# Performance work log

Hardware: AMD Instinct MI355X
Metric: run time of the kernel (lower is better)

Reference implementation:

```python
import jax, jax.numpy as jnp
import numpy as np

N_NODES = 100000
N_EDGES = 1200000
D = 64
N_CLASSES = 16
L2_EPS = 1e-12  # F.normalize default eps


def setup_inputs() -> dict:
    key = jax.random.key(0)
    ks = jax.random.split(key, 8)
    x = jax.random.normal(ks[0], (N_NODES, D), dtype=jnp.float32)
    src = jax.random.randint(ks[1], (N_EDGES,), 0, N_NODES, dtype=jnp.int32)
    dst = jax.random.randint(ks[2], (N_EDGES,), 0, N_NODES, dtype=jnp.int32)
    s = 1.0 / np.sqrt(D)
    W0 = jax.random.normal(ks[3], (D, D), dtype=jnp.float32) * s  # stored as [in, out]
    W1 = jax.random.normal(ks[4], (D, D), dtype=jnp.float32) * s
    W2 = jax.random.normal(ks[5], (D, D), dtype=jnp.float32) * s
    W_out = jax.random.normal(ks[6], (D, N_CLASSES), dtype=jnp.float32) * s
    b_out = jnp.zeros((N_CLASSES,), dtype=jnp.float32)
    return {"x": x, "src": src, "dst": dst, "W0": W0, "W1": W1, "W2": W2,
            "W_out": W_out, "b_out": b_out}


def reference(x, src, dst, W0, W1, W2, W_out, b_out):
    n = x.shape[0]
    h = x
    for W in (W0, W1, W2):
        # GINConv sum aggregation (eps=0): h_dst = h + sum over incoming edges
        agg = jax.ops.segment_sum(h[src], dst, num_segments=n)
        # MLP: relu(linear); GraphConv post-activation relu is idempotent on relu output
        h = jax.nn.relu((h + agg) @ W)
    # F.normalize: L2 row normalization with eps clamp
    norm = jnp.linalg.norm(h, axis=1, keepdims=True)
    feat = h / jnp.maximum(norm, L2_EPS)
    out = feat @ W_out + b_out
    return out, feat
```

## Files before the change

kernel.cpp:

```cpp
#include <hip/hip_runtime.h>
#include <hip/hip_fp16.h>

#define N_NODES 100000
#define N_EDGES 1200000
#define D 64
#define N_CLASSES 16
#define NG8  (N_NODES / 8)
#define GRID 2048
#define NXCD 8
#define DRANGE ((N_NODES + NXCD - 1) / NXCD)
#define ESRC_CAP 1900032
#define SENTINEL N_NODES
#define NB_CVT 6250
#define NRB 1024
#define RW 98
#define RCAP 2048
#define K1CH 1024
#define K1B ((N_EDGES / 4 + K1CH - 1) / K1CH)

typedef _Float16 f16x8 __attribute__((ext_vector_type(8)));
typedef float    f32x4 __attribute__((ext_vector_type(4)));

__global__ __launch_bounds__(256) void bucket_nr_kernel(
        const int* __restrict__ src,
        const int* __restrict__ dst,
        int* __restrict__ bcur,
        int* __restrict__ bpk) {
    __shared__ int hist[NRB];
    __shared__ int lofs[NRB + 1];
    __shared__ int gbase[NRB];
    __shared__ int tsum[256];
    __shared__ int pk[K1CH * 4];
    int tid = threadIdx.x;
    for (int i = tid; i < NRB; i += 256) hist[i] = 0;
    __syncthreads();

    int c0 = blockIdx.x * K1CH;
    int bn_rk[4][4], pkv[4][4];
#pragma unroll
    for (int it = 0; it < 4; ++it) {
        int c = c0 + it * 256 + tid;
        if (c < N_EDGES / 4) {
            int4 s4 = ((const int4*)src)[c];
            int4 d4 = ((const int4*)dst)[c];
            int ss[4] = {s4.x, s4.y, s4.z, s4.w};
            int dd[4] = {d4.x, d4.y, d4.z, d4.w};
#pragma unroll
            for (int j = 0; j < 4; ++j) {
                int b = dd[j] / RW;
                int rk = atomicAdd(&hist[b], 1);
                bn_rk[it][j] = (b << 16) | rk;
                pkv[it][j] = (ss[j] << 7) | (dd[j] - b * RW);
            }
        } else {
#pragma unroll
            for (int j = 0; j < 4; ++j) bn_rk[it][j] = -1;
        }
    }
    __syncthreads();
    int b4 = tid * 4;
    int h0 = hist[b4], h1 = hist[b4 + 1], h2 = hist[b4 + 2], h3 = hist[b4 + 3];
    int hs = h0 + h1 + h2 + h3;
    tsum[tid] = hs;
    __syncthreads();
    for (int d = 1; d < 256; d <<= 1) {
        int t = (tid >= d) ? tsum[tid - d] : 0;
        __syncthreads();
        tsum[tid] += t;
        __syncthreads();
    }
    int ex = tsum[tid] - hs;
    lofs[b4] = ex; lofs[b4 + 1] = ex + h0;
    lofs[b4 + 2] = ex + h0 + h1; lofs[b4 + 3] = ex + h0 + h1 + h2;
    if (tid == 255) lofs[NRB] = tsum[255];
    for (int b = tid; b < NRB; b += 256) {
        int cb = hist[b];
        gbase[b] = cb ? atomicAdd(&bcur[b], cb) : 0;
    }
    __syncthreads();
#pragma unroll
    for (int it = 0; it < 4; ++it)
#pragma unroll
        for (int j = 0; j < 4; ++j) {
            int br = bn_rk[it][j];
            if (br >= 0)
                pk[lofs[br >> 16] + (br & 0xffff)] = pkv[it][j];
        }
    __syncthreads();
    int total = lofs[NRB];
    for (int i = tid; i < total; i += 256) {
        int lo = 0, hi = NRB;
        while (hi - lo > 1) {
            int mid = (lo + hi) >> 1;
            if (lofs[mid] <= i) lo = mid; else hi = mid;
        }
        int pos = gbase[lo] + (i - lofs[lo]);
        if (pos < RCAP) bpk[lo * RCAP + pos] = pk[i];
    }
}

__global__ __launch_bounds__(256) void hist_nr_kernel(
        const int* __restrict__ bcur,
        const int* __restrict__ bpk,
        int* __restrict__ cnt) {
    __shared__ int lh[RW];
    int r = blockIdx.x, tid = threadIdx.x;
    if (tid < RW) lh[tid] = 0;
    __syncthreads();
    int nb = min(bcur[r], RCAP);
    const int* p = bpk + r * RCAP;
    for (int i = tid; i < nb; i += 256)
        atomicAdd(&lh[p[i] & 127], 1);
    __syncthreads();
    int n = r * RW + tid;
    if (tid < RW && n < N_NODES) cnt[n] = lh[tid];
}

__global__ void scan_block_kernel(const int* __restrict__ cnt,
                                  int* __restrict__ ofs,
                                  int* __restrict__ partial) {
    __shared__ int s[256];
    int tid = threadIdx.x;
    int i = blockIdx.x * 256 + tid;
    int v = (i < N_NODES) ? ((cnt[i] + 7) & ~7) : 0;
    s[tid] = v;
    __syncthreads();
    for (int d = 1; d < 256; d <<= 1) {
        int t = (tid >= d) ? s[tid - d] : 0;
        __syncthreads();
        s[tid] += t;
        __syncthreads();
    }
    if (i < N_NODES) ofs[i] = s[tid] - v;
    if (tid == 255) partial[blockIdx.x] = s[255];
}

__global__ void scan_partials_kernel(int* __restrict__ partial, int nb) {
    __shared__ int s[512];
    int tid = threadIdx.x;
    int v = (tid < nb) ? partial[tid] : 0;
    s[tid] = v;
    __syncthreads();
    for (int d = 1; d < 512; d <<= 1) {
        int t = (tid >= d) ? s[tid - d] : 0;
        __syncthreads();
        s[tid] += t;
        __syncthreads();
    }
    if (tid < nb) partial[tid] = s[tid] - v;
}

__global__ void scan_add_kernel(int* __restrict__ ofs,
                                const int* __restrict__ partial,
                                const int* __restrict__ cnt,
                                int* __restrict__ esrc) {
    int i = blockIdx.x * 256 + threadIdx.x;
    if (i < N_NODES) {
        int o = ofs[i] + partial[blockIdx.x];
        ofs[i] = o;
        int c = cnt[i], p = (c + 7) & ~7;
        for (int j = c; j < p; ++j) esrc[o + j] = SENTINEL;
        if (i == N_NODES - 1) ofs[N_NODES] = o + p;
    }
}

__global__ __launch_bounds__(256) void place_nr_kernel(
        const int* __restrict__ bcur,
        const int* __restrict__ bpk,
        const int* __restrict__ ofs,
        int* __restrict__ esrc) {
    __shared__ int lof[RW];
    __shared__ int lcur[RW];
    int r = blockIdx.x, tid = threadIdx.x;
    int n = r * RW + tid;
    if (tid < RW) {
        lof[tid] = (n < N_NODES) ? ofs[n] : 0;
        lcur[tid] = 0;
    }
    __syncthreads();
    int nb = min(bcur[r], RCAP);
    const int* p = bpk + r * RCAP;
    for (int i = tid; i < nb; i += 256) {
        int v = p[i];
        int dl = v & 127;
        int rk = atomicAdd(&lcur[dl], 1);
        esrc[lof[dl] + rk] = (unsigned)v >> 7;
    }
}

__global__ __launch_bounds__(256) void hist_kernel(const int* __restrict__ dst,
                                                   int* __restrict__ cnt) {
    int g = blockIdx.x & (NXCD - 1);
    int lo = g * DRANGE, hi = lo + DRANGE;
    int t = (blockIdx.x >> 3) * 256 + threadIdx.x;
    const int NCH = N_EDGES / 4;
    const int STRIDE = (GRID / NXCD) * 256;
    for (int c = t; c < NCH; c += STRIDE) {
        int4 d4 = ((const int4*)dst)[c];
        if (d4.x >= lo && d4.x < hi) atomicAdd(&cnt[d4.x], 1);
        if (d4.y >= lo && d4.y < hi) atomicAdd(&cnt[d4.y], 1);
        if (d4.z >= lo && d4.z < hi) atomicAdd(&cnt[d4.z], 1);
        if (d4.w >= lo && d4.w < hi) atomicAdd(&cnt[d4.w], 1);
    }
}

__global__ __launch_bounds__(256) void scatter_edges_kernel(
        const int* __restrict__ src,
        const int* __restrict__ dst,
        const int* __restrict__ ofs,
        int* __restrict__ cnt,
        int* __restrict__ esrc) {
    int g = blockIdx.x & (NXCD - 1);
    int lo = g * DRANGE, hi = lo + DRANGE;
    int t = (blockIdx.x >> 3) * 256 + threadIdx.x;
    const int NCH = N_EDGES / 4;
    const int STRIDE = (GRID / NXCD) * 256;
    for (int c = t; c < NCH; c += STRIDE) {
        int4 s4 = ((const int4*)src)[c];
        int4 d4 = ((const int4*)dst)[c];
        if (d4.x >= lo && d4.x < hi) esrc[ofs[d4.x] + atomicSub(&cnt[d4.x], 1) - 1] = s4.x;
        if (d4.y >= lo && d4.y < hi) esrc[ofs[d4.y] + atomicSub(&cnt[d4.y], 1) - 1] = s4.y;
        if (d4.z >= lo && d4.z < hi) esrc[ofs[d4.z] + atomicSub(&cnt[d4.z], 1) - 1] = s4.z;
        if (d4.w >= lo && d4.w < hi) esrc[ofs[d4.w] + atomicSub(&cnt[d4.w], 1) - 1] = s4.w;
    }
}

__global__ void prep_kernel(const float* __restrict__ x,
                            const float* __restrict__ W0,
                            const float* __restrict__ W1,
                            const float* __restrict__ W2,
                            __half* __restrict__ x16,
                            __half* __restrict__ w16,
                            __half* __restrict__ bufA,
                            __half* __restrict__ bufB) {
    int b = blockIdx.x;
    if (b < NB_CVT) {
        int i = b * 256 + threadIdx.x;
        float4 v = ((const float4*)x)[i];
        ((__half2*)x16)[2 * i + 0] = __floats2half2_rn(v.x, v.y);
        ((__half2*)x16)[2 * i + 1] = __floats2half2_rn(v.z, v.w);
    } else if (b < NB_CVT + 3) {
        int l = b - NB_CVT;
        const float* W = (l == 0) ? W0 : (l == 1) ? W1 : W2;
        for (int j = threadIdx.x; j < D * D; j += 256)
            w16[l * D * D + j] = __float2half(W[j]);
    } else {
        int tid = threadIdx.x;
        if (tid < 96) {
            __half* p = (tid < 32) ? x16 : (tid < 64) ? bufA : bufB;
            ((unsigned int*)(p + SENTINEL * D))[tid & 31] = 0u;
        }
    }
}

__global__ __launch_bounds__(256) void gather_kernel(
        const __half* __restrict__ h_in,
        const int* __restrict__ ofs,
        const int* __restrict__ esrc,
        __half* __restrict__ s_out) {
    int w = threadIdx.x >> 6, lane = threadIdx.x & 63;
    int q = lane >> 4;
    int c4 = lane & 15;
    int n = blockIdx.x * 16 + w * 4 + q;
    const uint2* hp = (const uint2*)h_in;

    uint2 self = hp[n * 16 + c4];
    float2 sl = __half22float2(*(const __half2*)&self.x);
    float2 sh = __half22float2(*(const __half2*)&self.y);
    float a0 = sl.x, a1 = sl.y, a2 = sh.x, a3 = sh.y;

    int k = ofs[n], end = ofs[n + 1];
    for (; k < end; k += 8) {
        int4 i0 = *(const int4*)(esrc + k);
        int4 i1 = *(const int4*)(esrc + k + 4);
        uint2 r0 = hp[i0.x * 16 + c4];
        uint2 r1 = hp[i0.y * 16 + c4];
        uint2 r2 = hp[i0.z * 16 + c4];
        uint2 r3 = hp[i0.w * 16 + c4];
        uint2 r4 = hp[i1.x * 16 + c4];
        uint2 r5 = hp[i1.y * 16 + c4];
        uint2 r6 = hp[i1.z * 16 + c4];
        uint2 r7 = hp[i1.w * 16 + c4];
#define ACC(R) { float2 lo = __half22float2(*(const __half2*)&R.x); \
                 float2 hi = __half22float2(*(const __half2*)&R.y); \
                 a0 += lo.x; a1 += lo.y; a2 += hi.x; a3 += hi.y; }
        ACC(r0) ACC(r1) ACC(r2) ACC(r3) ACC(r4) ACC(r5) ACC(r6) ACC(r7)
#undef ACC
    }
    uint2 ov;
    *(__half2*)&ov.x = __floats2half2_rn(a0, a1);
    *(__half2*)&ov.y = __floats2half2_rn(a2, a3);
    ((uint2*)s_out)[n * 16 + c4] = ov;
}

__global__ __launch_bounds__(256) void mlp_kernel(
        const __half* __restrict__ S,
        const __half* __restrict__ W16,
        __half* __restrict__ h_out) {
    int w = threadIdx.x >> 6, lane = threadIdx.x & 63;
    int m = lane & 15;
    int kg = lane >> 4;
    const _Float16* Wp = (const _Float16*)W16;
    f16x8 bf[4][2];
#pragma unroll
    for (int ct = 0; ct < 4; ++ct)
#pragma unroll
        for (int kt = 0; kt < 2; ++kt)
#pragma unroll
            for (int j = 0; j < 8; ++j)
                bf[ct][kt][j] = Wp[(kt * 32 + kg * 8 + j) * D + ct * 16 + m];

    int t = blockIdx.x * 4 + w;
    if (t >= N_NODES / 16) return;
    const _Float16* Sp = (const _Float16*)S;
    int row = t * 16 + m;
    f16x8 a0 = *(const f16x8*)(Sp + row * D + kg * 8);
    f16x8 a1 = *(const f16x8*)(Sp + row * D + 32 + kg * 8);
    f32x4 c[4];
#pragma unroll
    for (int ct = 0; ct < 4; ++ct) {
        f32x4 z = {0.f, 0.f, 0.f, 0.f};
        z = __builtin_amdgcn_mfma_f32_16x16x32_f16(a0, bf[ct][0], z, 0, 0, 0);
        z = __builtin_amdgcn_mfma_f32_16x16x32_f16(a1, bf[ct][1], z, 0, 0, 0);
        c[ct] = z;
    }
#pragma unroll
    for (int ct = 0; ct < 4; ++ct)
#pragma unroll
        for (int r = 0; r < 4; ++r)
            h_out[(t * 16 + kg * 4 + r) * D + ct * 16 + m] =
                __float2half(fmaxf(c[ct][r], 0.f));
}

__global__ __launch_bounds__(256) void final_kernel(
        const __half* __restrict__ h,
        const float* __restrict__ W_out,
        const float* __restrict__ b_out,
        float* __restrict__ out,
        float* __restrict__ feat) {
    __shared__ float Wo[D][N_CLASSES];
    __shared__ float fs[4][2][D];
    int tid = threadIdx.x;
    for (int k = tid; k < D * N_CLASSES; k += 256)
        Wo[k >> 4][k & 15] = W_out[k];
    __syncthreads();
    int w = tid >> 6;
    int lane = tid & 63;
    int hh = lane >> 5;
    int c2 = lane & 31;
    const __half2* hp = (const __half2*)h;
    float bias = b_out[lane & 15];

    for (int g = blockIdx.x; g < NG8; g += GRID) {
        int n = g * 8 + w * 2 + hh;
        float2 v = __half22float2(hp[n * 32 + c2]);
        float ss = v.x * v.x + v.y * v.y;
#pragma unroll
        for (int off = 16; off; off >>= 1)
            ss += __shfl_xor(ss, off);
        float rinv = 1.f / fmaxf(sqrtf(ss), 1e-12f);
        float f0 = v.x * rinv, f1 = v.y * rinv;
        ((float2*)feat)[n * 32 + c2] = make_float2(f0, f1);
        fs[w][hh][2 * c2 + 0] = f0;
        fs[w][hh][2 * c2 + 1] = f1;
        if (c2 < N_CLASSES) {
            float acc = bias;
#pragma unroll
            for (int i = 0; i < D; ++i)
                acc = fmaf(fs[w][hh][i], Wo[i][c2], acc);
            out[n * N_CLASSES + c2] = acc;
        }
    }
}

extern "C" void kernel_launch(void* const* d_in, const int* in_sizes, int n_in,
                              void* d_out, int out_size, void* d_ws, size_t ws_size,
                              hipStream_t stream) {
    const float* x     = (const float*)d_in[0];
    const int*   src   = (const int*)d_in[1];
    const int*   dst   = (const int*)d_in[2];
    const float* W0    = (const float*)d_in[3];
    const float* W1    = (const float*)d_in[4];
    const float* W2    = (const float*)d_in[5];
    const float* W_out = (const float*)d_in[6];
    const float* b_out = (const float*)d_in[7];

    float* out  = (float*)d_out;
    float* feat = (float*)d_out + (size_t)N_NODES * N_CLASSES;

    const int NB_NODE = (N_NODES + 255) / 256;
    const int NB_MLP  = (N_NODES / 16 + 3) / 4;

    size_t off = 0;
    auto alloc = [&](size_t bytes) { size_t o = off; off = (off + bytes + 255) & ~(size_t)255; return o; };
    size_t o_cnt     = alloc((size_t)N_NODES * 4);
    size_t o_partial = alloc(512 * 4);
    size_t o_ofs     = alloc(((size_t)N_NODES + 1) * 4);
    size_t o_esrc    = alloc((size_t)ESRC_CAP * 4);
    size_t o_w16     = alloc((size_t)3 * D * D * 2);
    size_t o_X       = alloc((size_t)(N_NODES + 1) * D * 2);
    size_t o_A       = alloc((size_t)(N_NODES + 1) * D * 2);
    size_t o_B       = alloc((size_t)(N_NODES + 1) * D * 2);
    size_t o_bcur    = alloc((size_t)NRB * 4);
    size_t o_bpk     = alloc((size_t)NRB * RCAP * 4);
    size_t need_bkt  = off;

    char* w8 = (char*)d_ws;
    int*    cnt     = (int*)(w8 + o_cnt);
    int*    partial = (int*)(w8 + o_partial);
    int*    ofs     = (int*)(w8 + o_ofs);
    int*    esrc    = (int*)(w8 + o_esrc);
    __half* w16     = (__half*)(w8 + o_w16);
    __half* X       = (__half*)(w8 + o_X);
    __half* A       = (__half*)(w8 + o_A);
    __half* B       = (__half*)(w8 + o_B);

    if (ws_size >= need_bkt) {
        int* bcur = (int*)(w8 + o_bcur);
        int* bpk  = (int*)(w8 + o_bpk);
        hipMemsetAsync(bcur, 0, (size_t)NRB * 4, stream);
        bucket_nr_kernel<<<K1B, 256, 0, stream>>>(src, dst, bcur, bpk);
        hist_nr_kernel<<<NRB, 256, 0, stream>>>(bcur, bpk, cnt);
        scan_block_kernel<<<NB_NODE, 256, 0, stream>>>(cnt, ofs, partial);
        scan_partials_kernel<<<1, 512, 0, stream>>>(partial, NB_NODE);
        scan_add_kernel<<<NB_NODE, 256, 0, stream>>>(ofs, partial, cnt, esrc);
        place_nr_kernel<<<NRB, 256, 0, stream>>>(bcur, bpk, ofs, esrc);
    } else {
        hipMemsetAsync(cnt, 0, (size_t)N_NODES * 4, stream);
        hist_kernel<<<GRID, 256, 0, stream>>>(dst, cnt);
        scan_block_kernel<<<NB_NODE, 256, 0, stream>>>(cnt, ofs, partial);
        scan_partials_kernel<<<1, 512, 0, stream>>>(partial, NB_NODE);
        scan_add_kernel<<<NB_NODE, 256, 0, stream>>>(ofs, partial, cnt, esrc);
        scatter_edges_kernel<<<GRID, 256, 0, stream>>>(src, dst, ofs, cnt, esrc);
    }

    prep_kernel<<<NB_CVT + 4, 256, 0, stream>>>(x, W0, W1, W2, X, w16, A, B);

    gather_kernel<<<N_NODES / 16, 256, 0, stream>>>(X, ofs, esrc, A);
    mlp_kernel<<<NB_MLP, 256, 0, stream>>>(A, w16 + 0 * D * D, B);
    gather_kernel<<<N_NODES / 16, 256, 0, stream>>>(B, ofs, esrc, X);
    mlp_kernel<<<NB_MLP, 256, 0, stream>>>(X, w16 + 1 * D * D, A);
    gather_kernel<<<N_NODES / 16, 256, 0, stream>>>(A, ofs, esrc, B);
    mlp_kernel<<<NB_MLP, 256, 0, stream>>>(B, w16 + 2 * D * D, X);

    final_kernel<<<GRID, 256, 0, stream>>>(X, W_out, b_out, out, feat);
}
```

Measured before the change: 192.3 us.

## Split node features into four 16-column chunks to shrink gather working set

Stores node feature buffers as four column chunks of 16 halves (32 bytes per node) instead of 128-byte rows. The gather kernel now processes one chunk per block, with 8 lanes per node and edge indices broadcast via shuffles. The MLP, prep and final kernels are updated to read and write the chunked layout. The intent is to make each gather pass touch a ~3.2 MB chunk that fits in cache better, in exchange for more gather blocks, rereading the edge lists once per chunk, and smaller 32-byte random accesses.

```diff
diff --git a/kernel.cpp b/kernel.cpp
--- a/kernel.cpp
+++ b/kernel.cpp
@@ -17,6 +17,11 @@
 #define RCAP 2048
 #define K1CH 1024
 #define K1B ((N_EDGES / 4 + K1CH - 1) / K1CH)
+#define NCHK 4
+#define CHS_H  ((N_NODES + 1) * 16)
+#define CHS_U  ((N_NODES + 1) * 8)
+#define CHS_H2 ((N_NODES + 1) * 8)
+#define NBC (N_NODES / 32)
 
 typedef _Float16 f16x8 __attribute__((ext_vector_type(8)));
 typedef float    f32x4 __attribute__((ext_vector_type(4)));
@@ -236,9 +241,13 @@
     int b = blockIdx.x;
     if (b < NB_CVT) {
         int i = b * 256 + threadIdx.x;
+        int n = i >> 4, j = i & 15;
         float4 v = ((const float4*)x)[i];
-        ((__half2*)x16)[2 * i + 0] = __floats2half2_rn(v.x, v.y);
-        ((__half2*)x16)[2 * i + 1] = __floats2half2_rn(v.z, v.w);
+        __half2 h01 = __floats2half2_rn(v.x, v.y);
+        __half2 h23 = __floats2half2_rn(v.z, v.w);
+        unsigned* hp = (unsigned*)x16 + (size_t)(j >> 2) * CHS_U + n * 8 + 2 * (j & 3);
+        hp[0] = *(unsigned*)&h01;
+        hp[1] = *(unsigned*)&h23;
     } else if (b < NB_CVT + 3) {
         int l = b - NB_CVT;
         const float* W = (l == 0) ? W0 : (l == 1) ? W1 : W2;
@@ -248,7 +257,8 @@
         int tid = threadIdx.x;
         if (tid < 96) {
             __half* p = (tid < 32) ? x16 : (tid < 64) ? bufA : bufB;
-            ((unsigned int*)(p + SENTINEL * D))[tid & 31] = 0u;
+            int t = tid & 31;
+            ((unsigned*)p)[(size_t)(t >> 3) * CHS_U + (size_t)SENTINEL * 8 + (t & 7)] = 0u;
         }
     }
 }
@@ -258,39 +268,38 @@
         const int* __restrict__ ofs,
         const int* __restrict__ esrc,
         __half* __restrict__ s_out) {
-    int w = threadIdx.x >> 6, lane = threadIdx.x & 63;
-    int q = lane >> 4;
-    int c4 = lane & 15;
-    int n = blockIdx.x * 16 + w * 4 + q;
-    const uint2* hp = (const uint2*)h_in;
-
-    uint2 self = hp[n * 16 + c4];
-    float2 sl = __half22float2(*(const __half2*)&self.x);
-    float2 sh = __half22float2(*(const __half2*)&self.y);
-    float a0 = sl.x, a1 = sl.y, a2 = sh.x, a3 = sh.y;
+    int c = blockIdx.x / NBC;
+    int nb = blockIdx.x - c * NBC;
+    int tid = threadIdx.x;
+    int g = tid >> 3;
+    int l = tid & 7;
+    int n = nb * 32 + g;
+    const unsigned* hp = (const unsigned*)h_in + (size_t)c * CHS_U;
+
+    unsigned selfv = hp[n * 8 + l];
+    float2 acc = __half22float2(*(__half2*)&selfv);
 
     int k = ofs[n], end = ofs[n + 1];
     for (; k < end; k += 8) {
-        int4 i0 = *(const int4*)(esrc + k);
-        int4 i1 = *(const int4*)(esrc + k + 4);
-        uint2 r0 = hp[i0.x * 16 + c4];
-        uint2 r1 = hp[i0.y * 16 + c4];
-        uint2 r2 = hp[i0.z * 16 + c4];
-        uint2 r3 = hp[i0.w * 16 + c4];
-        uint2 r4 = hp[i1.x * 16 + c4];
-        uint2 r5 = hp[i1.y * 16 + c4];
-        uint2 r6 = hp[i1.z * 16 + c4];
-        uint2 r7 = hp[i1.w * 16 + c4];
-#define ACC(R) { float2 lo = __half22float2(*(const __half2*)&R.x); \
-                 float2 hi = __half22float2(*(const __half2*)&R.y); \
-                 a0 += lo.x; a1 += lo.y; a2 += hi.x; a3 += hi.y; }
+        int idx = esrc[k + l];
+        int s0 = __shfl(idx, 0, 8), s1 = __shfl(idx, 1, 8);
+        int s2 = __shfl(idx, 2, 8), s3 = __shfl(idx, 3, 8);
+        int s4 = __shfl(idx, 4, 8), s5 = __shfl(idx, 5, 8);
+        int s6 = __shfl(idx, 6, 8), s7 = __shfl(idx, 7, 8);
+        unsigned r0 = hp[s0 * 8 + l];
+        unsigned r1 = hp[s1 * 8 + l];
+        unsigned r2 = hp[s2 * 8 + l];
+        unsigned r3 = hp[s3 * 8 + l];
+        unsigned r4 = hp[s4 * 8 + l];
+        unsigned r5 = hp[s5 * 8 + l];
+        unsigned r6 = hp[s6 * 8 + l];
+        unsigned r7 = hp[s7 * 8 + l];
+#define ACC(R) { float2 q = __half22float2(*(__half2*)&R); acc.x += q.x; acc.y += q.y; }
         ACC(r0) ACC(r1) ACC(r2) ACC(r3) ACC(r4) ACC(r5) ACC(r6) ACC(r7)
 #undef ACC
     }
-    uint2 ov;
-    *(__half2*)&ov.x = __floats2half2_rn(a0, a1);
-    *(__half2*)&ov.y = __floats2half2_rn(a2, a3);
-    ((uint2*)s_out)[n * 16 + c4] = ov;
+    __half2 hv = __floats2half2_rn(acc.x, acc.y);
+    ((unsigned*)s_out)[(size_t)c * CHS_U + n * 8 + l] = *(unsigned*)&hv;
 }
 
 __global__ __launch_bounds__(256) void mlp_kernel(
@@ -314,8 +323,8 @@
     if (t >= N_NODES / 16) return;
     const _Float16* Sp = (const _Float16*)S;
     int row = t * 16 + m;
-    f16x8 a0 = *(const f16x8*)(Sp + row * D + kg * 8);
-    f16x8 a1 = *(const f16x8*)(Sp + row * D + 32 + kg * 8);
+    f16x8 a0 = *(const f16x8*)(Sp + (size_t)(kg >> 1) * CHS_H + row * 16 + (kg & 1) * 8);
+    f16x8 a1 = *(const f16x8*)(Sp + (size_t)((kg >> 1) + 2) * CHS_H + row * 16 + (kg & 1) * 8);
     f32x4 c[4];
 #pragma unroll
     for (int ct = 0; ct < 4; ++ct) {
@@ -328,8 +337,8 @@
     for (int ct = 0; ct < 4; ++ct)
 #pragma unroll
         for (int r = 0; r < 4; ++r)
-            h_out[(t * 16 + kg * 4 + r) * D + ct * 16 + m] =
-                __float2half(fmaxf(c[ct][r], 0.f));
+            ((_Float16*)h_out)[(size_t)ct * CHS_H + (t * 16 + kg * 4 + r) * 16 + m] =
+                (_Float16)fmaxf(c[ct][r], 0.f);
 }
 
 __global__ __launch_bounds__(256) void final_kernel(
@@ -348,27 +357,28 @@
     int lane = tid & 63;
     int hh = lane >> 5;
     int c2 = lane & 31;
+    int ch = (c2 >> 3) * 16 + (c2 & 7) * 2;
     const __half2* hp = (const __half2*)h;
     float bias = b_out[lane & 15];
 
     for (int g = blockIdx.x; g < NG8; g += GRID) {
         int n = g * 8 + w * 2 + hh;
-        float2 v = __half22float2(hp[n * 32 + c2]);
+        float2 v = __half22float2(hp[(size_t)(c2 >> 3) * CHS_H2 + n * 8 + (c2 & 7)]);
         float ss = v.x * v.x + v.y * v.y;
 #pragma unroll
         for (int off = 16; off; off >>= 1)
             ss += __shfl_xor(ss, off);
         float rinv = 1.f / fmaxf(sqrtf(ss), 1e-12f);
         float f0 = v.x * rinv, f1 = v.y * rinv;
-        ((float2*)feat)[n * 32 + c2] = make_float2(f0, f1);
-        fs[w][hh][2 * c2 + 0] = f0;
-        fs[w][hh][2 * c2 + 1] = f1;
+        *(float2*)&feat[(size_t)n * D + ch] = make_float2(f0, f1);
+        fs[w][hh][ch + 0] = f0;
+        fs[w][hh][ch + 1] = f1;
         if (c2 < N_CLASSES) {
             float acc = bias;
 #pragma unroll
             for (int i = 0; i < D; ++i)
                 acc = fmaf(fs[w][hh][i], Wo[i][c2], acc);
-            out[n * N_CLASSES + c2] = acc;
+            out[(size_t)n * N_CLASSES + c2] = acc;
         }
     }
 }
@@ -398,9 +408,9 @@
     size_t o_ofs     = alloc(((size_t)N_NODES + 1) * 4);
     size_t o_esrc    = alloc((size_t)ESRC_CAP * 4);
     size_t o_w16     = alloc((size_t)3 * D * D * 2);
-    size_t o_X       = alloc((size_t)(N_NODES + 1) * D * 2);
-    size_t o_A       = alloc((size_t)(N_NODES + 1) * D * 2);
-    size_t o_B       = alloc((size_t)(N_NODES + 1) * D * 2);
+    size_t o_X       = alloc((size_t)NCHK * CHS_H * 2);
+    size_t o_A       = alloc((size_t)NCHK * CHS_H * 2);
+    size_t o_B       = alloc((size_t)NCHK * CHS_H * 2);
     size_t o_bcur    = alloc((size_t)NRB * 4);
     size_t o_bpk     = alloc((size_t)NRB * RCAP * 4);
     size_t need_bkt  = off;
@@ -436,11 +446,11 @@
 
     prep_kernel<<<NB_CVT + 4, 256, 0, stream>>>(x, W0, W1, W2, X, w16, A, B);
 
-    gather_kernel<<<N_NODES / 16, 256, 0, stream>>>(X, ofs, esrc, A);
+    gather_kernel<<<NCHK * NBC, 256, 0, stream>>>(X, ofs, esrc, A);
     mlp_kernel<<<NB_MLP, 256, 0, stream>>>(A, w16 + 0 * D * D, B);
-    gather_kernel<<<N_NODES / 16, 256, 0, stream>>>(B, ofs, esrc, X);
+    gather_kernel<<<NCHK * NBC, 256, 0, stream>>>(B, ofs, esrc, X);
     mlp_kernel<<<NB_MLP, 256, 0, stream>>>(X, w16 + 1 * D * D, A);
-    gather_kernel<<<N_NODES / 16, 256, 0, stream>>>(A, ofs, esrc, B);
+    gather_kernel<<<NCHK * NBC, 256, 0, stream>>>(A, ofs, esrc, B);
     mlp_kernel<<<NB_MLP, 256, 0, stream>>>(B, w16 + 2 * D * D, X);
 
     final_kernel<<<GRID, 256, 0, stream>>>(X, W_out, b_out, out, feat);
```

Result: slower. 222.5 us (+15.7%).

## Sort nodes into degree bins so gather wavefronts process similar-degree nodes

Applied to the files above, without the earlier changes.

Adds a degree histogram, scan and permutation pass that groups nodes by in-degree (in bins of eight edges), and makes the gather kernel process nodes in that permuted order. Each wavefront holds four nodes that loop over their edge lists in steps of eight, so grouping similar degrees is meant to reduce divergence where short-list nodes idle while long-list nodes finish. The cost is three extra small kernels and a memset, one extra indirection per node in gather, and writes to s_out that are now scattered rather than contiguous.

```diff
diff --git a/kernel.cpp b/kernel.cpp
--- a/kernel.cpp
+++ b/kernel.cpp
@@ -17,6 +17,7 @@
 #define RCAP 2048
 #define K1CH 1024
 #define K1B ((N_EDGES / 4 + K1CH - 1) / K1CH)
+#define DBINS 16
 
 typedef _Float16 f16x8 __attribute__((ext_vector_type(8)));
 typedef float    f32x4 __attribute__((ext_vector_type(4)));
@@ -185,6 +186,49 @@
         int dl = v & 127;
         int rk = atomicAdd(&lcur[dl], 1);
         esrc[lof[dl] + rk] = (unsigned)v >> 7;
+    }
+}
+
+__global__ void hist_deg_kernel(const int* __restrict__ cnt, int* __restrict__ gd) {
+    __shared__ int lh[DBINS];
+    int tid = threadIdx.x;
+    if (tid < DBINS) lh[tid] = 0;
+    __syncthreads();
+    int i = blockIdx.x * 256 + tid;
+    if (i < N_NODES) atomicAdd(&lh[min((cnt[i] + 7) >> 3, DBINS - 1)], 1);
+    __syncthreads();
+    if (tid < DBINS && lh[tid]) atomicAdd(&gd[tid], lh[tid]);
+}
+
+__global__ void scan_deg_kernel(int* __restrict__ gd) {
+    if (threadIdx.x == 0) {
+        int acc = 0;
+        for (int b = 0; b < DBINS; ++b) { int v = gd[b]; gd[DBINS + b] = acc; acc += v; }
+    }
+}
+
+__global__ void perm_kernel(const int* __restrict__ cnt,
+                            int* __restrict__ gd,
+                            int* __restrict__ perm) {
+    __shared__ int lh[DBINS], lbase[DBINS];
+    int tid = threadIdx.x;
+    if (tid < DBINS) lh[tid] = 0;
+    __syncthreads();
+    int i = blockIdx.x * 256 + tid;
+    int b = -1;
+    if (i < N_NODES) {
+        b = min((cnt[i] + 7) >> 3, DBINS - 1);
+        atomicAdd(&lh[b], 1);
+    }
+    __syncthreads();
+    if (tid < DBINS) {
+        lbase[tid] = lh[tid] ? atomicAdd(&gd[DBINS + tid], lh[tid]) : 0;
+        lh[tid] = 0;
+    }
+    __syncthreads();
+    if (i < N_NODES) {
+        int r = atomicAdd(&lh[b], 1);
+        perm[lbase[b] + r] = i;
     }
 }
 
@@ -223,6 +267,11 @@
         if (d4.z >= lo && d4.z < hi) esrc[ofs[d4.z] + atomicSub(&cnt[d4.z], 1) - 1] = s4.z;
         if (d4.w >= lo && d4.w < hi) esrc[ofs[d4.w] + atomicSub(&cnt[d4.w], 1) - 1] = s4.w;
     }
+}
+
+__global__ void iota_kernel(int* __restrict__ perm) {
+    int i = blockIdx.x * 256 + threadIdx.x;
+    if (i < N_NODES) perm[i] = i;
 }
 
 __global__ void prep_kernel(const float* __restrict__ x,
@@ -257,11 +306,12 @@
         const __half* __restrict__ h_in,
         const int* __restrict__ ofs,
         const int* __restrict__ esrc,
+        const int* __restrict__ perm,
         __half* __restrict__ s_out) {
     int w = threadIdx.x >> 6, lane = threadIdx.x & 63;
     int q = lane >> 4;
     int c4 = lane & 15;
-    int n = blockIdx.x * 16 + w * 4 + q;
+    int n = perm[blockIdx.x * 16 + w * 4 + q];
     const uint2* hp = (const uint2*)h_in;
 
     uint2 self = hp[n * 16 + c4];
@@ -401,6 +451,8 @@
     size_t o_X       = alloc((size_t)(N_NODES + 1) * D * 2);
     size_t o_A       = alloc((size_t)(N_NODES + 1) * D * 2);
     size_t o_B       = alloc((size_t)(N_NODES + 1) * D * 2);
+    size_t o_perm    = alloc((size_t)N_NODES * 4);
+    size_t o_gd      = alloc((size_t)2 * DBINS * 4);
     size_t o_bcur    = alloc((size_t)NRB * 4);
     size_t o_bpk     = alloc((size_t)NRB * RCAP * 4);
     size_t need_bkt  = off;
@@ -414,17 +466,23 @@
     __half* X       = (__half*)(w8 + o_X);
     __half* A       = (__half*)(w8 + o_A);
     __half* B       = (__half*)(w8 + o_B);
+    int*    perm    = (int*)(w8 + o_perm);
+    int*    gd      = (int*)(w8 + o_gd);
 
     if (ws_size >= need_bkt) {
         int* bcur = (int*)(w8 + o_bcur);
         int* bpk  = (int*)(w8 + o_bpk);
         hipMemsetAsync(bcur, 0, (size_t)NRB * 4, stream);
+        hipMemsetAsync(gd, 0, (size_t)2 * DBINS * 4, stream);
         bucket_nr_kernel<<<K1B, 256, 0, stream>>>(src, dst, bcur, bpk);
         hist_nr_kernel<<<NRB, 256, 0, stream>>>(bcur, bpk, cnt);
         scan_block_kernel<<<NB_NODE, 256, 0, stream>>>(cnt, ofs, partial);
         scan_partials_kernel<<<1, 512, 0, stream>>>(partial, NB_NODE);
         scan_add_kernel<<<NB_NODE, 256, 0, stream>>>(ofs, partial, cnt, esrc);
         place_nr_kernel<<<NRB, 256, 0, stream>>>(bcur, bpk, ofs, esrc);
+        hist_deg_kernel<<<NB_NODE, 256, 0, stream>>>(cnt, gd);
+        scan_deg_kernel<<<1, 64, 0, stream>>>(gd);
+        perm_kernel<<<NB_NODE, 256, 0, stream>>>(cnt, gd, perm);
     } else {
         hipMemsetAsync(cnt, 0, (size_t)N_NODES * 4, stream);
         hist_kernel<<<GRID, 256, 0, stream>>>(dst, cnt);
@@ -432,15 +490,16 @@
         scan_partials_kernel<<<1, 512, 0, stream>>>(partial, NB_NODE);
         scan_add_kernel<<<NB_NODE, 256, 0, stream>>>(ofs, partial, cnt, esrc);
         scatter_edges_kernel<<<GRID, 256, 0, stream>>>(src, dst, ofs, cnt, esrc);
+        iota_kernel<<<NB_NODE, 256, 0, stream>>>(perm);
     }
 
     prep_kernel<<<NB_CVT + 4, 256, 0, stream>>>(x, W0, W1, W2, X, w16, A, B);
 
-    gather_kernel<<<N_NODES / 16, 256, 0, stream>>>(X, ofs, esrc, A);
+    gather_kernel<<<N_NODES / 16, 256, 0, stream>>>(X, ofs, esrc, perm, A);
     mlp_kernel<<<NB_MLP, 256, 0, stream>>>(A, w16 + 0 * D * D, B);
-    gather_kernel<<<N_NODES / 16, 256, 0, stream>>>(B, ofs, esrc, X);
+    gather_kernel<<<N_NODES / 16, 256, 0, stream>>>(B, ofs, esrc, perm, X);
     mlp_kernel<<<NB_MLP, 256, 0, stream>>>(X, w16 + 1 * D * D, A);
-    gather_kernel<<<N_NODES / 16, 256, 0, stream>>>(A, ofs, esrc, B);
+    gather_kernel<<<N_NODES / 16, 256, 0, stream>>>(A, ofs, esrc, perm, B);
     mlp_kernel<<<NB_MLP, 256, 0, stream>>>(B, w16 + 2 * D * D, X);
 
     final_kernel<<<GRID, 256, 0, stream>>>(X, W_out, b_out, out, feat);
```

Measured after the change: 209.3 us. 1.09x slower.
